# Optimization experiments

Measured on AMD Instinct MI355X. Metric: run time of the kernel, lower is better.

## Reference

```python
import jax, jax.numpy as jnp
import numpy as np

K = 8          # number of nearest neighbors (init kwarg k)
EPS = 1e-16    # torch_geometric clamps squared distance at 1e-16


def setup_inputs() -> dict:
    key = jax.random.key(0)
    k1, k2, k3, k4 = jax.random.split(key, 4)
    N, D, B = 16384, 128, 64
    x1 = jax.random.normal(k1, (N, 3 + D), dtype=jnp.float32)  # true graph: [coords(3) | feats(D)]
    x2 = jax.random.normal(k2, (N, 3 + D), dtype=jnp.float32)  # pred graph
    b1 = jnp.sort(jax.random.randint(k3, (N,), 0, B))          # sorted per-node graph ids
    b2 = jnp.sort(jax.random.randint(k4, (N,), 0, B))
    return {"x1": x1, "x2": x2, "b1": b1, "b2": b2}


def _knn_interpolate(f1, c1, c2, b1, b2, k):
    # Squared pairwise distances [N2, N1] via ||a||^2 + ||b||^2 - 2ab (GEMM form).
    d2 = (jnp.sum(c2 * c2, axis=-1)[:, None]
          + jnp.sum(c1 * c1, axis=-1)[None, :]
          - 2.0 * (c2 @ c1.T))
    d2 = jnp.maximum(d2, 0.0)
    # Batch-aware kNN: forbid cross-graph neighbors.
    d2 = jnp.where(b2[:, None] != b1[None, :], jnp.inf, d2)
    neg_d2, idx = jax.lax.top_k(-d2, k)          # k smallest distances per target node
    w = 1.0 / jnp.clip(-neg_d2, EPS)             # [N2, k] inverse-squared-distance weights
    nbr = f1[idx]                                # [N2, k, D] gather of neighbor features
    return jnp.einsum('nk,nkd->nd', w, nbr) / jnp.sum(w, axis=-1, keepdims=True)


def reference(x1, x2, b1, b2):
    c1, f1 = x1[:, :3], x1[:, 3:]
    c2, f2 = x2[:, :3], x2[:, 3:]
    f1_interp = _knn_interpolate(f1, c1, c2, b1, b2, K)
    return jnp.mean((f1_interp - f2) ** 2)
```

## Files before the change

kernel.cpp:

```cpp
#include <hip/hip_runtime.h>
#include <math.h>

#define KNN 8
#define QPB 32
#define SUB 16
#define BLK 512
#define CAP 1024

__launch_bounds__(BLK, 4)
__global__ void knn_one(const float* __restrict__ x1,
                        const float* __restrict__ x2,
                        const int* __restrict__ b1,
                        const int* __restrict__ b2,
                        int N, int ROW, float scale,
                        unsigned long long* __restrict__ slot,
                        float* __restrict__ out) {
  __shared__ float4 c4[CAP];
  __shared__ int   bs[CAP];
  __shared__ int   s_info[2];
  __shared__ float2 nbrs[QPB][KNN];
  __shared__ float wred[BLK / 64];

  const int nwg = (int)gridDim.x;
  const int xcd = (int)blockIdx.x & 7, pos = (int)blockIdx.x >> 3;
  const int q8 = nwg >> 3, r8 = nwg & 7;
  const int bid = (xcd < r8) ? xcd * (q8 + 1) + pos
                             : r8 * (q8 + 1) + (xcd - r8) * q8 + pos;

  const int tid  = threadIdx.x;
  const int lane = tid & 63;
  const int wv   = tid >> 6;
  const int qi   = tid >> 4;
  const int sub  = tid & (SUB - 1);
  const int q0   = bid * QPB;
  const int q    = min(q0 + qi, N - 1);
  const int qlast = min(q0 + QPB - 1, N - 1);

  if (wv < 2) {
    const int bb = (wv == 0) ? b2[q0] : b2[qlast];
    const int target = bb + wv;
    int lo = 0, hi = N;
    while (lo < hi) {
      int step = (hi - lo + 63) >> 6;
      int p = lo + lane * step;
      bool pred = (p < hi) && (b1[p] < target);
      int c = __popcll(__ballot(pred));
      if (c == 0) { hi = lo; break; }
      int nlo = lo + (c - 1) * step + 1;
      hi = min(hi, lo + c * step);
      lo = nlo;
    }
    if (lane == 0) s_info[wv] = lo;
  }

  float qx, qy, qz; int mybatch;
  {
    const float* c2 = x2 + (size_t)q * ROW;
    qx = c2[0]; qy = c2[1]; qz = c2[2];
    mybatch = b2[q];
  }
  const float n2 = qx * qx + qy * qy + qz * qz;

  float dist[KNN]; int nidx[KNN];
#pragma unroll
  for (int k = 0; k < KNN; ++k) { dist[k] = INFINITY; nidx[k] = 0; }

  __syncthreads();
  const int s1v = s_info[0], e1v = s_info[1];

  for (int t0 = s1v; t0 < e1v; t0 += CAP) {
    const int t1 = min(t0 + CAP, e1v);
    __syncthreads();
    for (int i = t0 + tid; i < t1; i += BLK) {
      const float* p = x1 + (size_t)i * ROW;
      float cx = p[0], cy = p[1], cz = p[2];
      c4[i - t0] = make_float4(cx, cy, cz, cx * cx + cy * cy + cz * cz);
      bs[i - t0] = b1[i];
    }
    __syncthreads();
    for (int j = t0 + sub; j < t1; j += SUB) {
      float4 c = c4[j - t0];
      int bv = bs[j - t0];
      float d = fmaxf(fmaf(-2.0f, fmaf(qx, c.x, fmaf(qy, c.y, qz * c.z)), n2 + c.w), 0.0f);
      d = (bv == mybatch) ? d : INFINITY;
      bool lt[KNN];
#pragma unroll
      for (int k = 0; k < KNN; ++k) lt[k] = d < dist[k];
#pragma unroll
      for (int k = KNN - 1; k > 0; --k) {
        dist[k] = lt[k - 1] ? dist[k - 1] : (lt[k] ? d : dist[k]);
        nidx[k] = lt[k - 1] ? nidx[k - 1] : (lt[k] ? j : nidx[k]);
      }
      dist[0] = lt[0] ? d : dist[0];
      nidx[0] = lt[0] ? j : nidx[0];
    }
  }

#pragma unroll
  for (int r = 0; r < KNN; ++r) {
    float hd = dist[0]; int hx = nidx[0];
    float bd = hd; int bi = hx;
#pragma unroll
    for (int m = 1; m <= 8; m <<= 1) {
      float od = __shfl_xor(bd, m); int oi = __shfl_xor(bi, m);
      if (od < bd || (od == bd && oi < bi)) { bd = od; bi = oi; }
    }
    if (hd == bd && hx == bi) {
#pragma unroll
      for (int k = 0; k < KNN - 1; ++k) { dist[k] = dist[k + 1]; nidx[k] = nidx[k + 1]; }
      dist[KNN - 1] = INFINITY; nidx[KNN - 1] = 0;
    }
    if (sub == r)
      nbrs[qi][r] = make_float2(bd, __int_as_float(bi));
  }
  __syncthreads();

  float pacc = 0.0f;
#pragma unroll
  for (int qq = 0; qq < QPB / (BLK / 64); ++qq) {
    const int lq = wv * (QPB / (BLK / 64)) + qq;
    const int gq = q0 + lq;
    if (gq < N) {
      const float4* pn = (const float4*)&nbrs[lq][0];
      float4 n01 = pn[0], n23 = pn[1], n45 = pn[2], n67 = pn[3];
      float dd[KNN] = {n01.x, n01.z, n23.x, n23.z, n45.x, n45.z, n67.x, n67.z};
      int   id[KNN] = {__float_as_int(n01.y), __float_as_int(n01.w),
                       __float_as_int(n23.y), __float_as_int(n23.w),
                       __float_as_int(n45.y), __float_as_int(n45.w),
                       __float_as_int(n67.y), __float_as_int(n67.w)};
      float w[KNN]; float sw = 0.0f;
#pragma unroll
      for (int r = 0; r < KNN; ++r) { w[r] = 1.0f / fmaxf(dd[r], 1e-16f); sw += w[r]; }
      float acc0 = 0.0f, acc1 = 0.0f;
#pragma unroll
      for (int r = 0; r < KNN; ++r) {
        const float* f = x1 + (size_t)id[r] * ROW + 3;
        acc0 = fmaf(w[r], f[lane], acc0);
        acc1 = fmaf(w[r], f[lane + 64], acc1);
      }
      const float* f2 = x2 + (size_t)gq * ROW + 3;
      float rinv = 1.0f / sw;
      float e0 = fmaf(acc0, rinv, -f2[lane]);
      float e1 = fmaf(acc1, rinv, -f2[lane + 64]);
      pacc += e0 * e0 + e1 * e1;
    }
  }
#pragma unroll
  for (int off = 32; off > 0; off >>= 1) pacc += __shfl_xor(pacc, off);
  if (lane == 0) wred[wv] = pacc;
  __syncthreads();

  if (tid == 0) {
    float s = 0.0f;
#pragma unroll
    for (int w = 0; w < BLK / 64; ++w) s += wred[w];
    unsigned long long v =
        ((unsigned long long)(0x5A000000u | (unsigned)bid) << 32) |
        (unsigned long long)__float_as_uint(s);
    __hip_atomic_store(&slot[bid], v, __ATOMIC_RELAXED,
                       __HIP_MEMORY_SCOPE_AGENT);
  }

  if (bid == 0 && wv == 0) {
    const int nblk = nwg;
    float s = 0.0f;
    for (int r = 0; r * 64 + lane < nblk; ++r) {
      int i = r * 64 + lane;
      unsigned tag = 0x5A000000u | (unsigned)i;
      unsigned long long x = __hip_atomic_load(&slot[i], __ATOMIC_RELAXED,
                                               __HIP_MEMORY_SCOPE_AGENT);
      while ((unsigned)(x >> 32) != tag) {
        __builtin_amdgcn_s_sleep(8);
        x = __hip_atomic_load(&slot[i], __ATOMIC_RELAXED,
                              __HIP_MEMORY_SCOPE_AGENT);
      }
      s += __uint_as_float((unsigned)x);
    }
#pragma unroll
    for (int off = 32; off > 0; off >>= 1) s += __shfl_xor(s, off);
    if (lane == 0) out[0] = s * scale;
  }
}

extern "C" void kernel_launch(void* const* d_in, const int* in_sizes, int n_in,
                              void* d_out, int out_size, void* d_ws, size_t ws_size,
                              hipStream_t stream) {
  const float* x1 = (const float*)d_in[0];
  const float* x2 = (const float*)d_in[1];
  const int* b1 = (const int*)d_in[2];
  const int* b2 = (const int*)d_in[3];
  int N = in_sizes[2];
  int ROW = in_sizes[0] / N;
  float* out = (float*)d_out;

  int blocks = (N + QPB - 1) / QPB;
  unsigned long long* slot = (unsigned long long*)d_ws;
  if (ws_size < (size_t)blocks * sizeof(unsigned long long)) return;

  float scale = 1.0f / ((float)N * (float)(ROW - 3));
  knn_one<<<blocks, BLK, 0, stream>>>(x1, x2, b1, b2, N, ROW, scale, slot, out);
}
```

Measured before the change: 27.30 us.

## Fuse neighbor gather into merge loop, drop shared-memory handoff and barrier

Each 16-lane query subgroup now gathers and accumulates neighbor features right after each merge round, with every lane handling 8 feature columns at stride 16. This removes the shared nbrs buffer, a __syncthreads, and the per-wave re-read of neighbor data. It also prefetches the query's own features before the batch-range search so that load overlaps the search. The cost is more registers per thread and feature loads that are less coalesced (16 lanes at stride 16 instead of 64 contiguous lanes).

```diff
diff --git a/kernel.cpp b/kernel.cpp
--- a/kernel.cpp
+++ b/kernel.cpp
@@ -18,7 +18,6 @@
   __shared__ float4 c4[CAP];
   __shared__ int   bs[CAP];
   __shared__ int   s_info[2];
-  __shared__ float2 nbrs[QPB][KNN];
   __shared__ float wred[BLK / 64];
 
   const int nwg = (int)gridDim.x;
@@ -36,6 +35,18 @@
   const int q    = min(q0 + qi, N - 1);
   const int qlast = min(q0 + QPB - 1, N - 1);
 
+  float qx, qy, qz; int mybatch;
+  float f2v[KNN];
+  {
+    const float* c2 = x2 + (size_t)q * ROW;
+    qx = c2[0]; qy = c2[1]; qz = c2[2];
+    mybatch = b2[q];
+    const float* f2 = c2 + 3 + sub;
+#pragma unroll
+    for (int t = 0; t < KNN; ++t) f2v[t] = f2[16 * t];
+  }
+  const float n2 = qx * qx + qy * qy + qz * qz;
+
   if (wv < 2) {
     const int bb = (wv == 0) ? b2[q0] : b2[qlast];
     const int target = bb + wv;
@@ -52,14 +63,6 @@
     }
     if (lane == 0) s_info[wv] = lo;
   }
-
-  float qx, qy, qz; int mybatch;
-  {
-    const float* c2 = x2 + (size_t)q * ROW;
-    qx = c2[0]; qy = c2[1]; qz = c2[2];
-    mybatch = b2[q];
-  }
-  const float n2 = qx * qx + qy * qy + qz * qz;
 
   float dist[KNN]; int nidx[KNN];
 #pragma unroll
@@ -96,6 +99,11 @@
     }
   }
 
+  float acc[KNN];
+#pragma unroll
+  for (int t = 0; t < KNN; ++t) acc[t] = 0.f;
+  float sw = 0.f;
+  const float* x1f = x1 + 3 + sub;
 #pragma unroll
   for (int r = 0; r < KNN; ++r) {
     float hd = dist[0]; int hx = nidx[0];
@@ -110,39 +118,20 @@
       for (int k = 0; k < KNN - 1; ++k) { dist[k] = dist[k + 1]; nidx[k] = nidx[k + 1]; }
       dist[KNN - 1] = INFINITY; nidx[KNN - 1] = 0;
     }
-    if (sub == r)
-      nbrs[qi][r] = make_float2(bd, __int_as_float(bi));
+    float w = 1.0f / fmaxf(bd, 1e-16f);
+    sw += w;
+    const float* f = x1f + (size_t)bi * ROW;
+#pragma unroll
+    for (int t = 0; t < KNN; ++t) acc[t] = fmaf(w, f[16 * t], acc[t]);
   }
-  __syncthreads();
 
   float pacc = 0.0f;
+  if (q0 + qi < N) {
+    float rinv = 1.0f / sw;
 #pragma unroll
-  for (int qq = 0; qq < QPB / (BLK / 64); ++qq) {
-    const int lq = wv * (QPB / (BLK / 64)) + qq;
-    const int gq = q0 + lq;
-    if (gq < N) {
-      const float4* pn = (const float4*)&nbrs[lq][0];
-      float4 n01 = pn[0], n23 = pn[1], n45 = pn[2], n67 = pn[3];
-      float dd[KNN] = {n01.x, n01.z, n23.x, n23.z, n45.x, n45.z, n67.x, n67.z};
-      int   id[KNN] = {__float_as_int(n01.y), __float_as_int(n01.w),
-                       __float_as_int(n23.y), __float_as_int(n23.w),
-                       __float_as_int(n45.y), __float_as_int(n45.w),
-                       __float_as_int(n67.y), __float_as_int(n67.w)};
-      float w[KNN]; float sw = 0.0f;
-#pragma unroll
-      for (int r = 0; r < KNN; ++r) { w[r] = 1.0f / fmaxf(dd[r], 1e-16f); sw += w[r]; }
-      float acc0 = 0.0f, acc1 = 0.0f;
-#pragma unroll
-      for (int r = 0; r < KNN; ++r) {
-        const float* f = x1 + (size_t)id[r] * ROW + 3;
-        acc0 = fmaf(w[r], f[lane], acc0);
-        acc1 = fmaf(w[r], f[lane + 64], acc1);
-      }
-      const float* f2 = x2 + (size_t)gq * ROW + 3;
-      float rinv = 1.0f / sw;
-      float e0 = fmaf(acc0, rinv, -f2[lane]);
-      float e1 = fmaf(acc1, rinv, -f2[lane + 64]);
-      pacc += e0 * e0 + e1 * e1;
+    for (int t = 0; t < KNN; ++t) {
+      float e = fmaf(acc[t], rinv, -f2v[t]);
+      pacc += e * e;
     }
   }
 #pragma unroll
```

Result: faster. 24.64 us (-9.8%).
